# Kernel tuning notes

Hardware: AMD Instinct MI355X
Metric: run time of the kernel (lower is better)

The kernel has to match this reference:

```python
import jax, jax.numpy as jnp
import numpy as np

H = 16  # num_heads

def setup_inputs() -> dict:
    key = jax.random.key(0)
    ks = jax.random.split(key, 5)
    d = 1024
    s = 0.02
    return {
        'x': jax.random.normal(ks[0], (2, 2048, d), jnp.float32),
        'Wq': jax.random.normal(ks[1], (d, d), jnp.float32) * s,
        'bq': jnp.zeros((d,), jnp.float32),
        'Wk': jax.random.normal(ks[2], (d, d), jnp.float32) * s,
        'bk': jnp.zeros((d,), jnp.float32),
        'Wv': jax.random.normal(ks[3], (d, d), jnp.float32) * s,
        'bv': jnp.zeros((d,), jnp.float32),
        'Wo': jax.random.normal(ks[4], (d, d), jnp.float32) * s,
        'bo': jnp.zeros((d,), jnp.float32),
        'ln_scale': jnp.ones((d,), jnp.float32),
        'ln_bias': jnp.zeros((d,), jnp.float32),
    }

def _layernorm(x, scale, bias, eps=1e-6):
    mu = jnp.mean(x, axis=-1, keepdims=True)
    var = jnp.var(x, axis=-1, keepdims=True)
    return (x - mu) * jax.lax.rsqrt(var + eps) * scale + bias

def reference(x, Wq, bq, Wk, bk, Wv, bv, Wo, bo, ln_scale, ln_bias):
    b, n, d = x.shape
    hd = d // H
    scale = hd ** -0.5
    residual = x
    xn = _layernorm(x, ln_scale, ln_bias)
    # QKV projections, split heads: [b, n, d] -> [b, H, n, hd]
    def split(y):
        return y.reshape(b, n, H, hd).transpose(0, 2, 1, 3)
    q = split(xn @ Wq + bq)
    k = split(xn @ Wk + bk)
    v = split(xn @ Wv + bv)
    attn = jnp.einsum('bhid,bhjd->bhij', q, k) * scale
    attn = jax.nn.softmax(attn, axis=-1)
    out = jnp.einsum('bhij,bhjd->bhid', attn, v)
    out = out.transpose(0, 2, 1, 3).reshape(b, n, d)
    out = out @ Wo + bo
    return out + residual
```

## Files before the change

### kernel.cpp

```cpp
#include <hip/hip_runtime.h>

typedef __bf16 bf16;
typedef __bf16 bf16x8 __attribute__((ext_vector_type(8)));
typedef float f32x4 __attribute__((ext_vector_type(4)));

#define D_MODEL 1024
#define SEQ 2048
#define NH 16
#define HD 64

#define GLD16(gp, lp) __builtin_amdgcn_global_load_lds( \
    (const __attribute__((address_space(1))) void*)(gp), \
    (__attribute__((address_space(3))) void*)(lp), 16, 0, 0)

__device__ __forceinline__ int sigp(int r) {
    return (r & 0x23) | ((r & 0x0C) << 1) | ((r & 0x10) >> 2);
}

__global__ __launch_bounds__(256) void ln_kernel(const float* __restrict__ x,
        const float* __restrict__ g, const float* __restrict__ bta,
        bf16* __restrict__ xnb) {
    int tok = blockIdx.x;
    const float* xr = x + (size_t)tok * D_MODEL;
    float v[4];
    float s = 0.f, ss = 0.f;
#pragma unroll
    for (int j = 0; j < 4; ++j) {
        int idx = threadIdx.x + j * 256;
        float t = xr[idx];
        v[j] = t; s += t; ss += t * t;
    }
#pragma unroll
    for (int m = 32; m; m >>= 1) { s += __shfl_xor(s, m, 64); ss += __shfl_xor(ss, m, 64); }
    __shared__ float red_s[4], red_ss[4];
    int w = threadIdx.x >> 6;
    if ((threadIdx.x & 63) == 0) { red_s[w] = s; red_ss[w] = ss; }
    __syncthreads();
    s  = red_s[0] + red_s[1] + red_s[2] + red_s[3];
    ss = red_ss[0] + red_ss[1] + red_ss[2] + red_ss[3];
    float mu  = s * (1.f / D_MODEL);
    float var = ss * (1.f / D_MODEL) - mu * mu;
    float rstd = rsqrtf(var + 1e-6f);
    bf16* orow = xnb + (size_t)tok * D_MODEL;
#pragma unroll
    for (int j = 0; j < 4; ++j) {
        int idx = threadIdx.x + j * 256;
        float xn = (v[j] - mu) * rstd * g[idx] + bta[idx];
        orow[idx] = (bf16)xn;
    }
}

__global__ __launch_bounds__(256) void transpose_kernel(const float* __restrict__ W0,
        const float* __restrict__ W1, const float* __restrict__ W2,
        const float* __restrict__ W3, bf16* __restrict__ wt) {
    __shared__ float tile[32][33];
    int mat = blockIdx.z;
    const float* W = mat == 0 ? W0 : mat == 1 ? W1 : mat == 2 ? W2 : W3;
    bf16* dst = wt + (size_t)mat * D_MODEL * D_MODEL;
    int k0 = blockIdx.x * 32, n0 = blockIdx.y * 32;
    int tx = threadIdx.x & 31, ty0 = threadIdx.x >> 5;
#pragma unroll
    for (int r = 0; r < 4; ++r) {
        int ty = ty0 + r * 8;
        tile[ty][tx] = W[(size_t)(k0 + ty) * D_MODEL + n0 + tx];
    }
    __syncthreads();
#pragma unroll
    for (int r = 0; r < 4; ++r) {
        int ty = ty0 + r * 8;
        dst[(size_t)(n0 + ty) * D_MODEL + k0 + tx] = (bf16)tile[tx][ty];
    }
}

__global__ __launch_bounds__(256) void qkv_gemm(const bf16* __restrict__ A,
        const bf16* __restrict__ Bt, const float* __restrict__ bq,
        const float* __restrict__ bk, const float* __restrict__ bv,
        bf16* __restrict__ qo, bf16* __restrict__ ko, bf16* __restrict__ vto) {
    __shared__ __align__(16) bf16 As[128 * 32];
    __shared__ __align__(16) bf16 Bs[128 * 32];
    int m0 = blockIdx.x * 128, n0 = blockIdx.y * 128;
    int tid = threadIdx.x;
    int w = tid >> 6, l = tid & 63, lm = l & 15, lq = l >> 4;
    int wm = (w >> 1) * 64, wn = (w & 1) * 64;
    f32x4 acc[4][4] = {};
    const bf16* ag = A  + (size_t)(m0 + w * 32 + (l >> 2)) * D_MODEL + (l & 3) * 8;
    const bf16* bg = Bt + (size_t)(n0 + w * 32 + (l >> 2)) * D_MODEL + (l & 3) * 8;
    bf16* asd = &As[(w * 32) * 32];
    bf16* bsd = &Bs[(w * 32) * 32];
    for (int k0 = 0; k0 < D_MODEL; k0 += 32) {
        GLD16(ag,                asd);
        GLD16(ag + 16 * D_MODEL, asd + 16 * 32);
        GLD16(bg,                bsd);
        GLD16(bg + 16 * D_MODEL, bsd + 16 * 32);
        ag += 32; bg += 32;
        __syncthreads();
        bf16x8 af[4], bf_[4];
#pragma unroll
        for (int f = 0; f < 4; ++f) af[f]  = *(const bf16x8*)&As[(wm + f * 16 + lm) * 32 + lq * 8];
#pragma unroll
        for (int f = 0; f < 4; ++f) bf_[f] = *(const bf16x8*)&Bs[(wn + f * 16 + lm) * 32 + lq * 8];
#pragma unroll
        for (int fm = 0; fm < 4; ++fm)
#pragma unroll
            for (int fn = 0; fn < 4; ++fn)
                acc[fm][fn] = __builtin_amdgcn_mfma_f32_16x16x32_bf16(af[fm], bf_[fn], acc[fm][fn], 0, 0, 0);
        __syncthreads();
    }
#pragma unroll
    for (int fn = 0; fn < 4; ++fn) {
        int n_g = n0 + wn + fn * 16 + lm;
        int mat = n_g >> 10, within = n_g & 1023;
        int h = within >> 6, hdp = within & 63;
        float bias = mat == 0 ? bq[within] : mat == 1 ? bk[within] : bv[within];
#pragma unroll
        for (int fm = 0; fm < 4; ++fm) {
#pragma unroll
            for (int r = 0; r < 4; ++r) {
                int m_g = m0 + wm + fm * 16 + lq * 4 + r;
                int b_ = m_g >> 11, i = m_g & 2047;
                int bh = b_ * NH + h;
                float val = acc[fm][fn][r] + bias;
                if (mat == 0)      qo [((size_t)bh * SEQ + i) * HD + hdp] = (bf16)(val * 0.180336888f);
                else if (mat == 1) ko [((size_t)bh * SEQ + i) * HD + hdp] = (bf16)val;
                else               vto[((size_t)bh * HD + hdp) * SEQ + i] = (bf16)val;
            }
        }
    }
}

__global__ __launch_bounds__(256) void attn_kernel(const bf16* __restrict__ q,
        const bf16* __restrict__ k, const bf16* __restrict__ vt,
        bf16* __restrict__ aout) {
    __shared__ __align__(16) bf16 Ks[2][64 * 64];
    __shared__ __align__(16) bf16 Vs[2][64 * 64];
    int i0 = blockIdx.x * 128;
    int bh = blockIdx.y;
    int tid = threadIdx.x;
    int w = tid >> 6, l = tid & 63, lm = l & 15, lq = l >> 4;
    const bf16* qb = q + (size_t)bh * SEQ * HD;
    const bf16* kb = k + (size_t)bh * SEQ * HD;
    const bf16* vb = vt + (size_t)bh * HD * SEQ;

    bf16x8 qf[2][2];
#pragma unroll
    for (int mf = 0; mf < 2; ++mf)
#pragma unroll
        for (int kc = 0; kc < 2; ++kc)
            qf[mf][kc] = *(const bf16x8*)(qb + (size_t)(i0 + w * 32 + mf * 16 + lm) * HD + kc * 32 + lq * 8);

    int r0 = w * 16 + (l >> 3), r1 = r0 + 8;
    int g = l & 7;
    const bf16* kp0 = kb + (size_t)sigp(r0) * HD + g * 8;
    const bf16* kp1 = kb + (size_t)sigp(r1) * HD + g * 8;
    const bf16* vp0 = vb + (size_t)r0 * SEQ + g * 8;
    const bf16* vp1 = vb + (size_t)r1 * SEQ + g * 8;
    int d0 = r0 * 64 + ((g ^ (r0 & 7)) * 8);
    int d1 = r1 * 64 + ((g ^ (r1 & 7)) * 8);

    uint4 kr0 = *(const uint4*)kp0, kr1 = *(const uint4*)kp1;
    uint4 vr0 = *(const uint4*)vp0, vr1 = *(const uint4*)vp1;
    kp0 += 64 * HD; kp1 += 64 * HD; vp0 += 64; vp1 += 64;

    f32x4 o[2][4] = {};
    float l_acc[2] = {0.f, 0.f};

    for (int j0 = 0; j0 < SEQ; j0 += 64) {
        int b = (j0 >> 6) & 1;
        *(uint4*)&Ks[b][d0] = kr0; *(uint4*)&Ks[b][d1] = kr1;
        *(uint4*)&Vs[b][d0] = vr0; *(uint4*)&Vs[b][d1] = vr1;
        if (j0 + 64 < SEQ) {
            kr0 = *(const uint4*)kp0; kr1 = *(const uint4*)kp1;
            vr0 = *(const uint4*)vp0; vr1 = *(const uint4*)vp1;
            kp0 += 64 * HD; kp1 += 64 * HD; vp0 += 64; vp1 += 64;
        }
        __syncthreads();
        f32x4 s[2][4] = {};
#pragma unroll
        for (int kc = 0; kc < 2; ++kc) {
#pragma unroll
            for (int nt = 0; nt < 4; ++nt) {
                int r = nt * 16 + lm;
                int gl = (kc * 4 + lq) ^ (lm & 7);
                bf16x8 kf = *(const bf16x8*)&Ks[b][r * 64 + gl * 8];
                s[0][nt] = __builtin_amdgcn_mfma_f32_16x16x32_bf16(kf, qf[0][kc], s[0][nt], 0, 0, 0);
                s[1][nt] = __builtin_amdgcn_mfma_f32_16x16x32_bf16(kf, qf[1][kc], s[1][nt], 0, 0, 0);
            }
        }
#pragma unroll
        for (int mf = 0; mf < 2; ++mf) {
            float psum = 0.f;
#pragma unroll
            for (int nt = 0; nt < 4; ++nt)
#pragma unroll
                for (int r = 0; r < 4; ++r) {
                    float p = exp2f(s[mf][nt][r]);
                    s[mf][nt][r] = p; psum += p;
                }
            l_acc[mf] += psum;
        }
#pragma unroll
        for (int kc = 0; kc < 2; ++kc) {
            bf16x8 pf[2];
#pragma unroll
            for (int mf = 0; mf < 2; ++mf)
#pragma unroll
                for (int jj = 0; jj < 8; ++jj)
                    pf[mf][jj] = (bf16)s[mf][2 * kc + (jj >> 2)][jj & 3];
#pragma unroll
            for (int nt = 0; nt < 4; ++nt) {
                int p = nt * 16 + lm;
                int gl = (kc * 4 + lq) ^ (lm & 7);
                bf16x8 vf = *(const bf16x8*)&Vs[b][p * 64 + gl * 8];
                o[0][nt] = __builtin_amdgcn_mfma_f32_16x16x32_bf16(pf[0], vf, o[0][nt], 0, 0, 0);
                o[1][nt] = __builtin_amdgcn_mfma_f32_16x16x32_bf16(pf[1], vf, o[1][nt], 0, 0, 0);
            }
        }
    }
    int b_ = bh >> 4, h = bh & 15;
#pragma unroll
    for (int mf = 0; mf < 2; ++mf) {
        l_acc[mf] += __shfl_xor(l_acc[mf], 16, 64);
        l_acc[mf] += __shfl_xor(l_acc[mf], 32, 64);
        float linv[4];
#pragma unroll
        for (int r = 0; r < 4; ++r)
            linv[r] = 1.f / __shfl(l_acc[mf], lq * 4 + r, 64);
#pragma unroll
        for (int nt = 0; nt < 4; ++nt) {
#pragma unroll
            for (int r = 0; r < 4; ++r) {
                int i = i0 + w * 32 + mf * 16 + lq * 4 + r;
                int tok = b_ * SEQ + i;
                aout[(size_t)tok * D_MODEL + h * HD + nt * 16 + lm] = (bf16)(o[mf][nt][r] * linv[r]);
            }
        }
    }
}

__global__ __launch_bounds__(256) void out_gemm(const bf16* __restrict__ A,
        const bf16* __restrict__ Bt, const float* __restrict__ bo,
        const float* __restrict__ resid, float* __restrict__ out) {
    __shared__ __align__(16) bf16 As[128 * 32];
    __shared__ __align__(16) bf16 Bs[128 * 32];
    int m0 = blockIdx.x * 128, n0 = blockIdx.y * 128;
    int tid = threadIdx.x;
    int w = tid >> 6, l = tid & 63, lm = l & 15, lq = l >> 4;
    int wm = (w >> 1) * 64, wn = (w & 1) * 64;
    f32x4 acc[4][4] = {};
    const bf16* ag = A  + (size_t)(m0 + w * 32 + (l >> 2)) * D_MODEL + (l & 3) * 8;
    const bf16* bg = Bt + (size_t)(n0 + w * 32 + (l >> 2)) * D_MODEL + (l & 3) * 8;
    bf16* asd = &As[(w * 32) * 32];
    bf16* bsd = &Bs[(w * 32) * 32];
    for (int k0 = 0; k0 < D_MODEL; k0 += 32) {
        GLD16(ag,                asd);
        GLD16(ag + 16 * D_MODEL, asd + 16 * 32);
        GLD16(bg,                bsd);
        GLD16(bg + 16 * D_MODEL, bsd + 16 * 32);
        ag += 32; bg += 32;
        __syncthreads();
        bf16x8 af[4], bf_[4];
#pragma unroll
        for (int f = 0; f < 4; ++f) af[f]  = *(const bf16x8*)&As[(wm + f * 16 + lm) * 32 + lq * 8];
#pragma unroll
        for (int f = 0; f < 4; ++f) bf_[f] = *(const bf16x8*)&Bs[(wn + f * 16 + lm) * 32 + lq * 8];
#pragma unroll
        for (int fm = 0; fm < 4; ++fm)
#pragma unroll
            for (int fn = 0; fn < 4; ++fn)
                acc[fm][fn] = __builtin_amdgcn_mfma_f32_16x16x32_bf16(af[fm], bf_[fn], acc[fm][fn], 0, 0, 0);
        __syncthreads();
    }
#pragma unroll
    for (int fn = 0; fn < 4; ++fn) {
        int n_g = n0 + wn + fn * 16 + lm;
        float bias = bo[n_g];
#pragma unroll
        for (int fm = 0; fm < 4; ++fm) {
#pragma unroll
            for (int r = 0; r < 4; ++r) {
                int m_g = m0 + wm + fm * 16 + lq * 4 + r;
                size_t idx = (size_t)m_g * D_MODEL + n_g;
                out[idx] = acc[fm][fn][r] + bias + resid[idx];
            }
        }
    }
}

extern "C" void kernel_launch(void* const* d_in, const int* in_sizes, int n_in,
                              void* d_out, int out_size, void* d_ws, size_t ws_size,
                              hipStream_t stream) {
    const float* x  = (const float*)d_in[0];
    const float* Wq = (const float*)d_in[1];
    const float* bq = (const float*)d_in[2];
    const float* Wk = (const float*)d_in[3];
    const float* bk = (const float*)d_in[4];
    const float* Wv = (const float*)d_in[5];
    const float* bv = (const float*)d_in[6];
    const float* Wo = (const float*)d_in[7];
    const float* bo = (const float*)d_in[8];
    const float* g  = (const float*)d_in[9];
    const float* bt = (const float*)d_in[10];
    (void)in_sizes; (void)n_in; (void)out_size; (void)ws_size;

    char* ws = (char*)d_ws;
    const size_t M8 = (size_t)8 << 20;
    bf16* xnb = (bf16*)(ws);
    bf16* wt  = (bf16*)(ws + M8);
    bf16* qb  = (bf16*)(ws + 2 * M8);
    bf16* kb  = (bf16*)(ws + 3 * M8);
    bf16* vtb = (bf16*)(ws + 4 * M8);
    bf16* ao  = xnb;
    float* out = (float*)d_out;

    ln_kernel<<<4096, 256, 0, stream>>>(x, g, bt, xnb);
    transpose_kernel<<<dim3(32, 32, 4), 256, 0, stream>>>(Wq, Wk, Wv, Wo, wt);
    qkv_gemm<<<dim3(32, 24), 256, 0, stream>>>(xnb, wt, bq, bk, bv, qb, kb, vtb);
    attn_kernel<<<dim3(16, 32), 256, 0, stream>>>(qb, kb, vtb, ao);
    out_gemm<<<dim3(32, 8), 256, 0, stream>>>(ao, wt + (size_t)3 * D_MODEL * D_MODEL, bo, x, out);
}
```

Measured before the change: 217.4 us.

## Pre-swizzle K and V into MFMA fragment layout and load directly to registers

The QKV projection epilogue now writes K and V-transposed tiles in a layout that matches the per-lane MFMA operand order, with K rows permuted via the inverse sigma map. The attention kernel drops its LDS staging and block barriers and loads each lane's K/V fragments straight from global memory into registers as contiguous 16-byte loads, prefetching the next K tile. This removes LDS traffic and __syncthreads. In exchange, every wave in a block now fetches the full K/V tiles from global/L2 itself instead of sharing them, the epilogue stores become more scattered, and register pressure rises.

```diff
diff --git a/kernel.cpp b/kernel.cpp
--- a/kernel.cpp
+++ b/kernel.cpp
@@ -13,8 +13,8 @@
     (const __attribute__((address_space(1))) void*)(gp), \
     (__attribute__((address_space(3))) void*)(lp), 16, 0, 0)
 
-__device__ __forceinline__ int sigp(int r) {
-    return (r & 0x23) | ((r & 0x0C) << 1) | ((r & 0x10) >> 2);
+__device__ __forceinline__ int sigi(int y) {
+    return (y & 0x23) | ((y & 0x18) >> 1) | ((y & 0x04) << 2);
 }
 
 __global__ __launch_bounds__(256) void ln_kernel(const float* __restrict__ x,
@@ -120,9 +120,23 @@
                 int b_ = m_g >> 11, i = m_g & 2047;
                 int bh = b_ * NH + h;
                 float val = acc[fm][fn][r] + bias;
-                if (mat == 0)      qo [((size_t)bh * SEQ + i) * HD + hdp] = (bf16)(val * 0.180336888f);
-                else if (mat == 1) ko [((size_t)bh * SEQ + i) * HD + hdp] = (bf16)val;
-                else               vto[((size_t)bh * HD + hdp) * SEQ + i] = (bf16)val;
+                if (mat == 0) {
+                    qo[((size_t)bh * SEQ + i) * HD + hdp] = (bf16)(val * 0.180336888f);
+                } else {
+                    int jt = i >> 6, jl = i & 63;
+                    if (mat == 1) {
+                        int idx = sigi(jl);
+                        int nt_ = idx >> 4, lm_ = idx & 15;
+                        int kc_ = hdp >> 5, lq_ = (hdp >> 3) & 3, e_ = hdp & 7;
+                        ko[(size_t)bh * SEQ * HD + (size_t)jt * 4096 +
+                           (kc_ * 4 + nt_) * 512 + (lq_ * 16 + lm_) * 8 + e_] = (bf16)val;
+                    } else {
+                        int nt_ = hdp >> 4, lm_ = hdp & 15;
+                        int kc_ = jl >> 5, lq_ = (jl >> 3) & 3, e_ = jl & 7;
+                        vto[(size_t)bh * SEQ * HD + (size_t)jt * 4096 +
+                            (kc_ * 4 + nt_) * 512 + (lq_ * 16 + lm_) * 8 + e_] = (bf16)val;
+                    }
+                }
             }
         }
     }
@@ -131,15 +145,13 @@
 __global__ __launch_bounds__(256) void attn_kernel(const bf16* __restrict__ q,
         const bf16* __restrict__ k, const bf16* __restrict__ vt,
         bf16* __restrict__ aout) {
-    __shared__ __align__(16) bf16 Ks[2][64 * 64];
-    __shared__ __align__(16) bf16 Vs[2][64 * 64];
     int i0 = blockIdx.x * 128;
     int bh = blockIdx.y;
     int tid = threadIdx.x;
     int w = tid >> 6, l = tid & 63, lm = l & 15, lq = l >> 4;
-    const bf16* qb = q + (size_t)bh * SEQ * HD;
-    const bf16* kb = k + (size_t)bh * SEQ * HD;
-    const bf16* vb = vt + (size_t)bh * HD * SEQ;
+    const bf16* qb = q  + (size_t)bh * SEQ * HD;
+    const bf16* kp = k  + (size_t)bh * SEQ * HD + l * 8;
+    const bf16* vp = vt + (size_t)bh * SEQ * HD + l * 8;
 
     bf16x8 qf[2][2];
 #pragma unroll
@@ -148,44 +160,42 @@
         for (int kc = 0; kc < 2; ++kc)
             qf[mf][kc] = *(const bf16x8*)(qb + (size_t)(i0 + w * 32 + mf * 16 + lm) * HD + kc * 32 + lq * 8);
 
-    int r0 = w * 16 + (l >> 3), r1 = r0 + 8;
-    int g = l & 7;
-    const bf16* kp0 = kb + (size_t)sigp(r0) * HD + g * 8;
-    const bf16* kp1 = kb + (size_t)sigp(r1) * HD + g * 8;
-    const bf16* vp0 = vb + (size_t)r0 * SEQ + g * 8;
-    const bf16* vp1 = vb + (size_t)r1 * SEQ + g * 8;
-    int d0 = r0 * 64 + ((g ^ (r0 & 7)) * 8);
-    int d1 = r1 * 64 + ((g ^ (r1 & 7)) * 8);
-
-    uint4 kr0 = *(const uint4*)kp0, kr1 = *(const uint4*)kp1;
-    uint4 vr0 = *(const uint4*)vp0, vr1 = *(const uint4*)vp1;
-    kp0 += 64 * HD; kp1 += 64 * HD; vp0 += 64; vp1 += 64;
+    bf16x8 kcur[2][4];
+#pragma unroll
+    for (int kc = 0; kc < 2; ++kc)
+#pragma unroll
+        for (int nt = 0; nt < 4; ++nt)
+            kcur[kc][nt] = *(const bf16x8*)(kp + (kc * 4 + nt) * 512);
+    kp += 4096;
 
     f32x4 o[2][4] = {};
     float l_acc[2] = {0.f, 0.f};
 
     for (int j0 = 0; j0 < SEQ; j0 += 64) {
-        int b = (j0 >> 6) & 1;
-        *(uint4*)&Ks[b][d0] = kr0; *(uint4*)&Ks[b][d1] = kr1;
-        *(uint4*)&Vs[b][d0] = vr0; *(uint4*)&Vs[b][d1] = vr1;
+        bf16x8 vcur[2][4];
+#pragma unroll
+        for (int kc = 0; kc < 2; ++kc)
+#pragma unroll
+            for (int nt = 0; nt < 4; ++nt)
+                vcur[kc][nt] = *(const bf16x8*)(vp + (kc * 4 + nt) * 512);
+        vp += 4096;
+        bf16x8 knxt[2][4];
         if (j0 + 64 < SEQ) {
-            kr0 = *(const uint4*)kp0; kr1 = *(const uint4*)kp1;
-            vr0 = *(const uint4*)vp0; vr1 = *(const uint4*)vp1;
-            kp0 += 64 * HD; kp1 += 64 * HD; vp0 += 64; vp1 += 64;
-        }
-        __syncthreads();
+#pragma unroll
+            for (int kc = 0; kc < 2; ++kc)
+#pragma unroll
+                for (int nt = 0; nt < 4; ++nt)
+                    knxt[kc][nt] = *(const bf16x8*)(kp + (kc * 4 + nt) * 512);
+            kp += 4096;
+        }
         f32x4 s[2][4] = {};
 #pragma unroll
-        for (int kc = 0; kc < 2; ++kc) {
+        for (int kc = 0; kc < 2; ++kc)
 #pragma unroll
             for (int nt = 0; nt < 4; ++nt) {
-                int r = nt * 16 + lm;
-                int gl = (kc * 4 + lq) ^ (lm & 7);
-                bf16x8 kf = *(const bf16x8*)&Ks[b][r * 64 + gl * 8];
-                s[0][nt] = __builtin_amdgcn_mfma_f32_16x16x32_bf16(kf, qf[0][kc], s[0][nt], 0, 0, 0);
-                s[1][nt] = __builtin_amdgcn_mfma_f32_16x16x32_bf16(kf, qf[1][kc], s[1][nt], 0, 0, 0);
-            }
-        }
+                s[0][nt] = __builtin_amdgcn_mfma_f32_16x16x32_bf16(kcur[kc][nt], qf[0][kc], s[0][nt], 0, 0, 0);
+                s[1][nt] = __builtin_amdgcn_mfma_f32_16x16x32_bf16(kcur[kc][nt], qf[1][kc], s[1][nt], 0, 0, 0);
+            }
 #pragma unroll
         for (int mf = 0; mf < 2; ++mf) {
             float psum = 0.f;
@@ -208,13 +218,15 @@
                     pf[mf][jj] = (bf16)s[mf][2 * kc + (jj >> 2)][jj & 3];
 #pragma unroll
             for (int nt = 0; nt < 4; ++nt) {
-                int p = nt * 16 + lm;
-                int gl = (kc * 4 + lq) ^ (lm & 7);
-                bf16x8 vf = *(const bf16x8*)&Vs[b][p * 64 + gl * 8];
-                o[0][nt] = __builtin_amdgcn_mfma_f32_16x16x32_bf16(pf[0], vf, o[0][nt], 0, 0, 0);
-                o[1][nt] = __builtin_amdgcn_mfma_f32_16x16x32_bf16(pf[1], vf, o[1][nt], 0, 0, 0);
-            }
-        }
+                o[0][nt] = __builtin_amdgcn_mfma_f32_16x16x32_bf16(pf[0], vcur[kc][nt], o[0][nt], 0, 0, 0);
+                o[1][nt] = __builtin_amdgcn_mfma_f32_16x16x32_bf16(pf[1], vcur[kc][nt], o[1][nt], 0, 0, 0);
+            }
+        }
+#pragma unroll
+        for (int kc = 0; kc < 2; ++kc)
+#pragma unroll
+            for (int nt = 0; nt < 4; ++nt)
+                kcur[kc][nt] = knxt[kc][nt];
     }
     int b_ = bh >> 4, h = bh & 15;
 #pragma unroll
```

Result: slower. 233.2 us (+7.3%).
